# Kernel tuning notes

Hardware: AMD Instinct MI355X
Metric: run time of the kernel (lower is better)

Reference implementation:

```python
import jax, jax.numpy as jnp
import numpy as np

BETA = 1e-8
ALPHA = 0.5
CHOOSE_K = 128
MEMORY_SIZE = 65536
KEY_DIM = 256
BATCH = 1024


def _l2norm(x, axis=-1, eps=1e-12):
    return x / jnp.sqrt(jnp.sum(x * x, axis=axis, keepdims=True) + eps)


def setup_inputs() -> dict:
    key = jax.random.key(0)
    k1, k2, k3 = jax.random.split(key, 3)
    q = _l2norm(jax.random.normal(k1, (BATCH, KEY_DIM), dtype=jnp.float32))
    memory_key = _l2norm(jax.random.normal(k2, (MEMORY_SIZE, KEY_DIM), dtype=jnp.float32))
    # module init: hist[:] = 1e-5; add small random variation so topk is non-degenerate
    memory_hist = 1e-5 + 1e-3 * jax.random.uniform(k3, (MEMORY_SIZE,), dtype=jnp.float32)
    # module init: values = ones, second half zeroed
    memory_values = jnp.concatenate([
        jnp.ones((MEMORY_SIZE // 2,), dtype=jnp.float32),
        jnp.zeros((MEMORY_SIZE - MEMORY_SIZE // 2,), dtype=jnp.float32),
    ])
    return {"q": q, "memory_key": memory_key,
            "memory_hist": memory_hist, "memory_values": memory_values}


def reference(q, memory_key, memory_hist, memory_values):
    # obtain_topk over FULL memory: dense similarity [B, M]
    sims = jnp.matmul(q, memory_key.T)                      # [B, M]
    scores = jnp.exp(sims - 1.0) * (memory_hist + BETA)[None, :]
    _, k_idxs = jax.lax.top_k(scores, CHOOSE_K)             # [B, K]

    # gather reduced memory at topk indices
    red_keys = memory_key[k_idxs]                           # [B, K, D]
    red_hist = memory_hist[k_idxs] * ALPHA                  # [B, K]
    red_vals = memory_values[k_idxs]                        # [B, K]

    # posterior over the K gathered slots
    sim_k = jnp.einsum('bd,bkd->bk', q, red_keys)           # [B, K]
    joint = jnp.exp(sim_k - 1.0) * (red_hist + BETA)        # [B, K]
    posterior = joint / jnp.sum(joint, axis=1, keepdims=True)
    result = jnp.sum(posterior * red_vals, axis=1)          # [B]
    return result
```

## Files before the change

kernel.cpp:

```cpp
#include <hip/hip_runtime.h>

#define BATCH   1024
#define MSIZE   65536
#define KDIM    256
#define CHOOSEK 128
#define SELK    160
#define CLCAP   2816
#define BETA    1e-8f
#define ALPHA   0.5f
#define KSC  425.0f
#define KOFF 7.2f

typedef short bf16x8 __attribute__((ext_vector_type(8)));
typedef float f32x4  __attribute__((ext_vector_type(4)));

__device__ inline unsigned int pack2bf(float a, float b) {
    unsigned int ua = __float_as_uint(a);
    unsigned int ub = __float_as_uint(b);
    ua += 0x7fffu + ((ua >> 16) & 1u);
    ub += 0x7fffu + ((ub >> 16) & 1u);
    return (ua >> 16) | (ub & 0xffff0000u);
}

#define GLD16(g, l) __builtin_amdgcn_global_load_lds( \
    (const __attribute__((address_space(1))) unsigned int*)(g), \
    (__attribute__((address_space(3))) unsigned int*)(l), 16, 0, 0)

__global__ __launch_bounds__(256)
void convert_kernel(const float* __restrict__ q, const float* __restrict__ key,
                    const float* __restrict__ hist,
                    unsigned short* __restrict__ qs, unsigned short* __restrict__ kb,
                    float* __restrict__ Ltab)
{
    const int bid = blockIdx.x, tid = threadIdx.x;
    if (bid < 8192) {
        const int off = bid * 256 + tid;
        const float4* s4 = (const float4*)key;
        float4 a = s4[off * 2], b = s4[off * 2 + 1];
        ((uint4*)kb)[off] = make_uint4(pack2bf(a.x, a.y), pack2bf(a.z, a.w),
                                       pack2bf(b.x, b.y), pack2bf(b.z, b.w));
    } else if (bid < 8320) {
        const int f = (bid - 8192) * 256 + tid;
        const int l = f & 63, j = (f >> 6) & 3, ks = (f >> 8) & 7;
        const int wmg = (f >> 11) & 3, bt = (f >> 13) & 3;
        const int r = bt * 256 + wmg * 64 + j * 16 + (l & 15);
        const int c = ks * 32 + (l >> 4) * 8;
        const float* src = q + (size_t)r * KDIM + c;
        float4 a = *(const float4*)src, b = *(const float4*)(src + 4);
        ((uint4*)qs)[f] = make_uint4(pack2bf(a.x, a.y), pack2bf(a.z, a.w),
                                     pack2bf(b.x, b.y), pack2bf(b.z, b.w));
    } else {
        const int n = (bid - 8320) * 256 + tid;
        Ltab[n] = (logf(hist[n] + BETA) + KOFF) * KSC;
    }
}

__global__ __launch_bounds__(512, 4)
void score_kernel(const unsigned short* __restrict__ qs,
                  const unsigned short* __restrict__ kb,
                  const float* __restrict__ Ltab,
                  unsigned char* __restrict__ s8,
                  unsigned long long* __restrict__ gmask)
{
    __shared__ __align__(16) unsigned short Bs[3][128 * 32];
    const int tid = threadIdx.x;
    const int bid = blockIdx.x;
    const int bt = (bid >> 3) & 3;
    const int b0 = bt * 256;
    const int n0 = ((bid & 7) + ((bid >> 5) << 3)) * 128;
    const int lane = tid & 63, wave = tid >> 6;
    const int wm = (wave >> 1) * 64, wn = (wave & 1) * 64;
    const int l15 = lane & 15, l4 = lane >> 4;
    const int wmg = wave >> 1;

    f32x4 acc[4][4] = {};

    const int srow = tid >> 2;
    const int seg  = (tid & 3) * 8;
    const unsigned short* gB = kb + (size_t)(n0 + srow) * KDIM + seg;
    const int lofs = srow * 32 + seg;

    const bf16x8* qw = (const bf16x8*)qs + (size_t)((bt * 4 + wmg) * 32) * 64 + lane;

    bf16x8 qf[2][4];

#define STAGE_B(st) GLD16(gB + (st) * 32, &Bs[(st) % 3][lofs])

#define STEP(s, WN) do {                                                          \
    asm volatile("s_waitcnt vmcnt(" #WN ")" ::: "memory");                        \
    __builtin_amdgcn_s_barrier();                                                 \
    asm volatile("" ::: "memory");                                                \
    if ((s) < 7) {                                                                \
        _Pragma("unroll")                                                         \
        for (int j = 0; j < 4; ++j)                                               \
            qf[((s) + 1) & 1][j] = qw[(((s) + 1) * 4 + j) * 64];                  \
    }                                                                             \
    if ((s) + 2 < 8) STAGE_B((s) + 2);                                            \
    bf16x8 kf[4];                                                                 \
    _Pragma("unroll")                                                             \
    for (int i = 0; i < 4; ++i)                                                   \
        kf[i] = *(const bf16x8*)(&Bs[(s) % 3][(wn + i * 16 + l15) * 32 + l4 * 8]);\
    __builtin_amdgcn_s_setprio(1);                                                \
    _Pragma("unroll")                                                             \
    for (int i = 0; i < 4; ++i)                                                   \
        _Pragma("unroll")                                                         \
        for (int j = 0; j < 4; ++j)                                               \
            acc[i][j] = __builtin_amdgcn_mfma_f32_16x16x32_bf16(kf[i], qf[(s) & 1][j], acc[i][j], 0, 0, 0); \
    __builtin_amdgcn_s_setprio(0);                                                \
} while (0)

#pragma unroll
    for (int j = 0; j < 4; ++j) qf[0][j] = qw[j * 64];
    STAGE_B(0); STAGE_B(1);

    STEP(0, 1); STEP(1, 1); STEP(2, 1); STEP(3, 1);
    STEP(4, 1); STEP(5, 1); STEP(6, 1); STEP(7, 0);

#undef STEP
#undef STAGE_B

    float4 Lv[4];
#pragma unroll
    for (int i = 0; i < 4; ++i)
        Lv[i] = *(const float4*)&Ltab[n0 + wn + i * 16 + l4 * 4];
#pragma unroll
    for (int j = 0; j < 4; ++j) {
        const int rb = b0 + wm + j * 16 + l15;
        const size_t row = (size_t)rb * MSIZE;
        unsigned int mlo = 0, mhi = 0;
#pragma unroll
        for (int i = 0; i < 4; ++i) {
            const float* lv = (const float*)&Lv[i];
            const int nb = n0 + wn + i * 16 + l4 * 4;
            unsigned int pk = 0;
#pragma unroll
            for (int reg = 0; reg < 4; ++reg) {
                float x = fmaf(acc[i][j][reg], KSC, lv[reg]);
                x = fminf(fmaxf(x, 0.0f), 255.0f);
                pk |= (unsigned int)(int)x << (8 * reg);
            }
            *(unsigned int*)(s8 + row + nb) = pk;
            unsigned int nib = ((pk >> 7) & 1u) | ((pk >> 14) & 2u) |
                               ((pk >> 21) & 4u) | ((pk >> 28) & 8u);
            if (i < 2) mlo |= nib << (i * 16 + l4 * 4);
            else       mhi |= nib << ((i - 2) * 16 + l4 * 4);
        }
        mlo |= __shfl_xor(mlo, 16, 64); mhi |= __shfl_xor(mhi, 16, 64);
        mlo |= __shfl_xor(mlo, 32, 64); mhi |= __shfl_xor(mhi, 32, 64);
        if (l4 == 0)
            gmask[(size_t)rb * (MSIZE / 64) + ((n0 + wn) >> 6)] =
                ((unsigned long long)mhi << 32) | mlo;
    }
}

__global__ __launch_bounds__(256, 4)
void select_kernel(const float* __restrict__ q,
                   const float* __restrict__ key,
                   const float* __restrict__ hist,
                   const float* __restrict__ vals,
                   const unsigned char* __restrict__ s8,
                   const unsigned long long* __restrict__ gmask,
                   float* __restrict__ out)
{
    const int b   = blockIdx.x;
    const int tid = threadIdx.x;

    __shared__ __align__(16) float qs[KDIM];
    __shared__ unsigned int hcnt[8 * 257];
    __shared__ int   stot[256];
    __shared__ int   scal[3];
    __shared__ unsigned int clist[CLCAP];
    __shared__ int   cidx[1024];
    __shared__ float csc[1024], cjj[1024], cjv[1024];
    __shared__ float wred[8];

    qs[tid] = q[(size_t)b * KDIM + tid];
    const unsigned char* s8row = s8 + (size_t)b * MSIZE;
    const unsigned long long* gm = gmask + (size_t)b * (MSIZE / 64);
    const int rep = (tid & 7) * 257;

    for (int i = tid; i < 8 * 257; i += 256) hcnt[i] = 0u;
    if (tid == 0) { scal[0] = -1; scal[1] = 0; scal[2] = 0; }
    __syncthreads();

    for (int k = tid; k < MSIZE / 64; k += 256) {
        unsigned long long m = gm[k];
        while (m) {
            int bpos = __builtin_ctzll(m);
            m &= m - 1;
            int idx = k * 64 + bpos;
            unsigned int by = s8row[idx];
            int p = atomicAdd(&scal[2], 1);
            if (p < CLCAP) clist[p] = (by << 16) | (unsigned int)idx;
            atomicAdd(&hcnt[rep + by], 1u);
        }
    }
    __syncthreads();
    const int ncl = scal[2];
    int mode = (ncl >= SELK && ncl <= CLCAP) ? 0 : 1;
    int H = -1;

    for (;;) {
        if (mode == 1) {
            __syncthreads();
            for (int i = tid; i < 8 * 257; i += 256) hcnt[i] = 0u;
            if (tid == 0) { scal[0] = -1; scal[1] = 0; }
            __syncthreads();
            const uint4* rowp = reinterpret_cast<const uint4*>(s8row);
            for (int i = 0; i < 16; ++i) {
                uint4 v = rowp[i * 256 + tid];
                unsigned int w[4] = {v.x, v.y, v.z, v.w};
#pragma unroll
                for (int k = 0; k < 4; ++k)
#pragma unroll
                    for (int jj = 0; jj < 4; ++jj)
                        atomicAdd(&hcnt[rep + ((w[k] >> (8 * jj)) & 0xffu)], 1u);
            }
            __syncthreads();
        }
        { unsigned int t = 0;
#pragma unroll
          for (int k = 0; k < 8; ++k) t += hcnt[k * 257 + tid];
          stot[tid] = (int)t; }
        __syncthreads();
        if (tid < 64) {
            const int l = tid;
            int t0 = stot[l * 4], t1 = stot[l * 4 + 1], t2 = stot[l * 4 + 2], t3 = stot[l * 4 + 3];
            int lsum = t0 + t1 + t2 + t3;
            int s = lsum;
#pragma unroll
            for (int off = 1; off < 64; off <<= 1) {
                int u = __shfl_down(s, off, 64);
                if (l + off < 64) s += u;
            }
            int A  = s - lsum;
            int S3 = A + t3;
            int S2 = S3 + t2;
            int S1 = S2 + t1;
            int S0 = S1 + t0;
            if (S0 >= SELK && S1 < SELK) scal[0] = l * 4 + 0;
            if (S1 >= SELK && S2 < SELK) scal[0] = l * 4 + 1;
            if (S2 >= SELK && S3 < SELK) scal[0] = l * 4 + 2;
            if (S3 >= SELK && A  < SELK) scal[0] = l * 4 + 3;
        }
        __syncthreads();
        H = scal[0];
        __syncthreads();
        if (H >= 0) break;
        mode = 1;
    }

    const unsigned int uH = (unsigned int)H;
    if (mode == 0) {
        for (int i = tid; i < ncl; i += 256) {
            unsigned int e = clist[i];
            if ((e >> 16) >= uH) {
                int p = atomicAdd(&scal[1], 1);
                if (p < 1024) cidx[p] = (int)(e & 0xffffu);
            }
        }
    } else {
        const uint4* rowp = reinterpret_cast<const uint4*>(s8row);
        for (int i = 0; i < 16; ++i) {
            uint4 v = rowp[i * 256 + tid];
            const int base = (i * 256 + tid) * 16;
            unsigned int w[4] = {v.x, v.y, v.z, v.w};
#pragma unroll
            for (int k = 0; k < 4; ++k)
#pragma unroll
                for (int jj = 0; jj < 4; ++jj) {
                    unsigned int bb = (w[k] >> (8 * jj)) & 0xffu;
                    if (bb >= uH) {
                        int p = atomicAdd(&scal[1], 1);
                        if (p < 1024) cidx[p] = base + 4 * k + jj;
                    }
                }
        }
    }
    __syncthreads();
    const int ncand = min(scal[1], 1024);

    const int gid = tid >> 4, gll = tid & 15;
    const float4* q4 = (const float4*)qs;
    for (int i = gid; i < ncand; i += 16) {
        const int idx = cidx[i];
        const float4* kp = (const float4*)(key + (size_t)idx * KDIM);
        float p = 0.f;
#pragma unroll
        for (int u = 0; u < 4; ++u) {
            float4 kk = kp[gll * 4 + u];
            float4 qq = q4[gll * 4 + u];
            p += kk.x * qq.x + kk.y * qq.y + kk.z * qq.z + kk.w * qq.w;
        }
#pragma unroll
        for (int off = 1; off < 16; off <<= 1) p += __shfl_xor(p, off, 64);
        if (gll == 0) {
            float e = expf(p - 1.0f);
            float h = hist[idx];
            csc[i] = e * (h + BETA);
            float j = e * (ALPHA * h + BETA);
            cjj[i] = j;
            cjv[i] = j * vals[idx];
        }
    }
    __syncthreads();

    const int wave = tid >> 6, lane = tid & 63;
    float pn = 0.f, pd = 0.f;
    for (int i = tid; i < ncand; i += 256) {
        float si = csc[i]; int ii = cidx[i]; int rank = 0;
        for (int t = 0; t < ncand; ++t) {
            float st = csc[t];
            rank += (st > si || (st == si && cidx[t] < ii)) ? 1 : 0;
        }
        if (rank < CHOOSEK) { pn += cjv[i]; pd += cjj[i]; }
    }
#pragma unroll
    for (int off = 32; off > 0; off >>= 1) {
        pn += __shfl_xor(pn, off, 64);
        pd += __shfl_xor(pd, off, 64);
    }
    if (lane == 0) { wred[wave] = pn; wred[4 + wave] = pd; }
    __syncthreads();
    if (tid == 0) {
        float n = wred[0] + wred[1] + wred[2] + wred[3];
        float d = wred[4] + wred[5] + wred[6] + wred[7];
        out[b] = n / d;
    }
}

extern "C" void kernel_launch(void* const* d_in, const int* in_sizes, int n_in,
                              void* d_out, int out_size, void* d_ws, size_t ws_size,
                              hipStream_t stream)
{
    (void)in_sizes; (void)n_in; (void)out_size; (void)ws_size;
    const float* q    = (const float*)d_in[0];
    const float* key  = (const float*)d_in[1];
    const float* hist = (const float*)d_in[2];
    const float* vals = (const float*)d_in[3];
    float* out = (float*)d_out;

    unsigned char*  s8 = (unsigned char*)d_ws;
    unsigned short* kb = (unsigned short*)((char*)d_ws + ((size_t)64 << 20));
    unsigned short* qsw= (unsigned short*)((char*)d_ws + ((size_t)96 << 20));
    float*          Lt = (float*)((char*)d_ws + ((size_t)96 << 20) + (512 << 10));
    unsigned long long* gmask = (unsigned long long*)((char*)d_ws + ((size_t)97 << 20));

    convert_kernel<<<8576, 256, 0, stream>>>(q, key, hist, qsw, kb, Lt);
    score_kernel<<<2048, 512, 0, stream>>>(qsw, kb, Lt, s8, gmask);
    select_kernel<<<BATCH, 256, 0, stream>>>(q, key, hist, vals, s8, gmask, out);
}
```

Baseline: 203.7 us.

## Process two N-tiles per score block, overlapping first epilogue with second tile prefetch

Each score_kernel block now handles two consecutive 128-column tiles of memory keys instead of one, halving the grid to 1024 blocks. The 3-stage LDS pipeline continues across the tile boundary, so the first tile's epilogue (byte quantization and mask writes) runs while loads for the second tile are already in flight. This is meant to amortize block launch and pipeline fill/drain costs, at the expense of fewer blocks for load balancing and some added register pressure.

```diff
diff --git a/kernel.cpp b/kernel.cpp
--- a/kernel.cpp
+++ b/kernel.cpp
@@ -67,7 +67,7 @@
     const int bid = blockIdx.x;
     const int bt = (bid >> 3) & 3;
     const int b0 = bt * 256;
-    const int n0 = ((bid & 7) + ((bid >> 5) << 3)) * 128;
+    const int n0 = ((bid & 7) + ((bid >> 5) << 3)) * 256;
     const int lane = tid & 63, wave = tid >> 6;
     const int wm = (wave >> 1) * 64, wn = (wave & 1) * 64;
     const int l15 = lane & 15, l4 = lane >> 4;
@@ -84,18 +84,19 @@
 
     bf16x8 qf[2][4];
 
-#define STAGE_B(st) GLD16(gB + (st) * 32, &Bs[(st) % 3][lofs])
+#define STAGE_B(st) GLD16(gB + ((st) >> 3) * 128 * KDIM + ((st) & 7) * 32, \
+                          &Bs[(st) % 3][lofs])
 
 #define STEP(s, WN) do {                                                          \
     asm volatile("s_waitcnt vmcnt(" #WN ")" ::: "memory");                        \
     __builtin_amdgcn_s_barrier();                                                 \
     asm volatile("" ::: "memory");                                                \
-    if ((s) < 7) {                                                                \
+    if ((s) < 15) {                                                               \
         _Pragma("unroll")                                                         \
         for (int j = 0; j < 4; ++j)                                               \
-            qf[((s) + 1) & 1][j] = qw[(((s) + 1) * 4 + j) * 64];                  \
+            qf[((s) + 1) & 1][j] = qw[((((s) + 1) & 7) * 4 + j) * 64];            \
     }                                                                             \
-    if ((s) + 2 < 8) STAGE_B((s) + 2);                                            \
+    if ((s) + 2 < 16) STAGE_B((s) + 2);                                           \
     bf16x8 kf[4];                                                                 \
     _Pragma("unroll")                                                             \
     for (int i = 0; i < 4; ++i)                                                   \
@@ -109,48 +110,64 @@
     __builtin_amdgcn_s_setprio(0);                                                \
 } while (0)
 
+#define EPI(T) do {                                                               \
+    float4 Lv[4];                                                                 \
+    _Pragma("unroll")                                                             \
+    for (int i = 0; i < 4; ++i)                                                   \
+        Lv[i] = *(const float4*)&Ltab[n0 + (T) * 128 + wn + i * 16 + l4 * 4];     \
+    _Pragma("unroll")                                                             \
+    for (int j = 0; j < 4; ++j) {                                                 \
+        const int rb = b0 + wm + j * 16 + l15;                                    \
+        const size_t row = (size_t)rb * MSIZE;                                    \
+        unsigned int mlo = 0, mhi = 0;                                            \
+        _Pragma("unroll")                                                         \
+        for (int i = 0; i < 4; ++i) {                                             \
+            const float* lv = (const float*)&Lv[i];                               \
+            const int nb = n0 + (T) * 128 + wn + i * 16 + l4 * 4;                 \
+            unsigned int pk = 0;                                                  \
+            _Pragma("unroll")                                                     \
+            for (int reg = 0; reg < 4; ++reg) {                                   \
+                float x = fmaf(acc[i][j][reg], KSC, lv[reg]);                     \
+                x = fminf(fmaxf(x, 0.0f), 255.0f);                                \
+                pk |= (unsigned int)(int)x << (8 * reg);                          \
+            }                                                                     \
+            *(unsigned int*)(s8 + row + nb) = pk;                                 \
+            unsigned int nib = ((pk >> 7) & 1u) | ((pk >> 14) & 2u) |             \
+                               ((pk >> 21) & 4u) | ((pk >> 28) & 8u);             \
+            if (i < 2) mlo |= nib << (i * 16 + l4 * 4);                           \
+            else       mhi |= nib << ((i - 2) * 16 + l4 * 4);                     \
+        }                                                                         \
+        mlo |= __shfl_xor(mlo, 16, 64); mhi |= __shfl_xor(mhi, 16, 64);           \
+        mlo |= __shfl_xor(mlo, 32, 64); mhi |= __shfl_xor(mhi, 32, 64);           \
+        if (l4 == 0)                                                              \
+            gmask[(size_t)rb * (MSIZE / 64) + ((n0 + (T) * 128 + wn) >> 6)] =     \
+                ((unsigned long long)mhi << 32) | mlo;                            \
+    }                                                                             \
+} while (0)
+
 #pragma unroll
     for (int j = 0; j < 4; ++j) qf[0][j] = qw[j * 64];
     STAGE_B(0); STAGE_B(1);
 
     STEP(0, 1); STEP(1, 1); STEP(2, 1); STEP(3, 1);
-    STEP(4, 1); STEP(5, 1); STEP(6, 1); STEP(7, 0);
-
+    STEP(4, 1); STEP(5, 1); STEP(6, 1); STEP(7, 1);
+
+    EPI(0);
+#pragma unroll
+    for (int i = 0; i < 4; ++i)
+#pragma unroll
+        for (int j = 0; j < 4; ++j)
+            acc[i][j] = (f32x4){0.f, 0.f, 0.f, 0.f};
+
+    STEP(8, 2);
+    STEP(9, 1); STEP(10, 1); STEP(11, 1); STEP(12, 1);
+    STEP(13, 1); STEP(14, 1); STEP(15, 0);
+
+    EPI(1);
+
+#undef EPI
 #undef STEP
 #undef STAGE_B
-
-    float4 Lv[4];
-#pragma unroll
-    for (int i = 0; i < 4; ++i)
-        Lv[i] = *(const float4*)&Ltab[n0 + wn + i * 16 + l4 * 4];
-#pragma unroll
-    for (int j = 0; j < 4; ++j) {
-        const int rb = b0 + wm + j * 16 + l15;
-        const size_t row = (size_t)rb * MSIZE;
-        unsigned int mlo = 0, mhi = 0;
-#pragma unroll
-        for (int i = 0; i < 4; ++i) {
-            const float* lv = (const float*)&Lv[i];
-            const int nb = n0 + wn + i * 16 + l4 * 4;
-            unsigned int pk = 0;
-#pragma unroll
-            for (int reg = 0; reg < 4; ++reg) {
-                float x = fmaf(acc[i][j][reg], KSC, lv[reg]);
-                x = fminf(fmaxf(x, 0.0f), 255.0f);
-                pk |= (unsigned int)(int)x << (8 * reg);
-            }
-            *(unsigned int*)(s8 + row + nb) = pk;
-            unsigned int nib = ((pk >> 7) & 1u) | ((pk >> 14) & 2u) |
-                               ((pk >> 21) & 4u) | ((pk >> 28) & 8u);
-            if (i < 2) mlo |= nib << (i * 16 + l4 * 4);
-            else       mhi |= nib << ((i - 2) * 16 + l4 * 4);
-        }
-        mlo |= __shfl_xor(mlo, 16, 64); mhi |= __shfl_xor(mhi, 16, 64);
-        mlo |= __shfl_xor(mlo, 32, 64); mhi |= __shfl_xor(mhi, 32, 64);
-        if (l4 == 0)
-            gmask[(size_t)rb * (MSIZE / 64) + ((n0 + wn) >> 6)] =
-                ((unsigned long long)mhi << 32) | mlo;
-    }
 }
 
 __global__ __launch_bounds__(256, 4)
@@ -347,6 +364,6 @@
     unsigned long long* gmask = (unsigned long long*)((char*)d_ws + ((size_t)97 << 20));
 
     convert_kernel<<<8576, 256, 0, stream>>>(q, key, hist, qsw, kb, Lt);
-    score_kernel<<<2048, 512, 0, stream>>>(qsw, kb, Lt, s8, gmask);
+    score_kernel<<<1024, 512, 0, stream>>>(qsw, kb, Lt, s8, gmask);
     select_kernel<<<BATCH, 256, 0, stream>>>(q, key, hist, vals, s8, gmask, out);
 }
```

After: 257.6 us. 26.5% more time.

## Use fixed-threshold bitmask directly as candidate list, skipping histogram in common path

Applied to the files above, without the earlier changes.

The GEMM epilogue now sets mask bits for quantized scores at or above a fixed threshold instead of the top bit. The select kernel counts mask bits with popcount and a wave reduction. When the count falls between SELK and 1024, it writes candidate indices straight from the mask using a per-thread atomic offset, with no byte histogram, threshold search or clist compaction. This cuts shared-memory atomics and a byte read per candidate. It relies on the fixed threshold giving a suitable candidate count and falls back to the full histogram path otherwise.

```diff
diff --git a/kernel.cpp b/kernel.cpp
--- a/kernel.cpp
+++ b/kernel.cpp
@@ -5,7 +5,7 @@
 #define KDIM    256
 #define CHOOSEK 128
 #define SELK    160
-#define CLCAP   2816
+#define MASKT   152
 #define BETA    1e-8f
 #define ALPHA   0.5f
 #define KSC  425.0f
@@ -132,16 +132,15 @@
         for (int i = 0; i < 4; ++i) {
             const float* lv = (const float*)&Lv[i];
             const int nb = n0 + wn + i * 16 + l4 * 4;
-            unsigned int pk = 0;
+            unsigned int pk = 0, nib = 0;
 #pragma unroll
             for (int reg = 0; reg < 4; ++reg) {
                 float x = fmaf(acc[i][j][reg], KSC, lv[reg]);
                 x = fminf(fmaxf(x, 0.0f), 255.0f);
                 pk |= (unsigned int)(int)x << (8 * reg);
+                nib |= (x >= (float)MASKT ? 1u : 0u) << reg;
             }
             *(unsigned int*)(s8 + row + nb) = pk;
-            unsigned int nib = ((pk >> 7) & 1u) | ((pk >> 14) & 2u) |
-                               ((pk >> 21) & 4u) | ((pk >> 28) & 8u);
             if (i < 2) mlo |= nib << (i * 16 + l4 * 4);
             else       mhi |= nib << ((i - 2) * 16 + l4 * 4);
         }
@@ -168,8 +167,7 @@
     __shared__ __align__(16) float qs[KDIM];
     __shared__ unsigned int hcnt[8 * 257];
     __shared__ int   stot[256];
-    __shared__ int   scal[3];
-    __shared__ unsigned int clist[CLCAP];
+    __shared__ int   scal[4];
     __shared__ int   cidx[1024];
     __shared__ float csc[1024], cjj[1024], cjv[1024];
     __shared__ float wred[8];
@@ -177,47 +175,51 @@
     qs[tid] = q[(size_t)b * KDIM + tid];
     const unsigned char* s8row = s8 + (size_t)b * MSIZE;
     const unsigned long long* gm = gmask + (size_t)b * (MSIZE / 64);
-    const int rep = (tid & 7) * 257;
-
-    for (int i = tid; i < 8 * 257; i += 256) hcnt[i] = 0u;
-    if (tid == 0) { scal[0] = -1; scal[1] = 0; scal[2] = 0; }
+
+    if (tid == 0) { scal[0] = -1; scal[1] = 0; scal[2] = 0; scal[3] = 0; }
     __syncthreads();
 
-    for (int k = tid; k < MSIZE / 64; k += 256) {
-        unsigned long long m = gm[k];
-        while (m) {
-            int bpos = __builtin_ctzll(m);
-            m &= m - 1;
-            int idx = k * 64 + bpos;
-            unsigned int by = s8row[idx];
-            int p = atomicAdd(&scal[2], 1);
-            if (p < CLCAP) clist[p] = (by << 16) | (unsigned int)idx;
-            atomicAdd(&hcnt[rep + by], 1u);
-        }
-    }
+    unsigned long long mw[4];
+    int myc = 0;
+#pragma unroll
+    for (int k = 0; k < 4; ++k) { mw[k] = gm[tid + k * 256]; myc += __popcll(mw[k]); }
+    { int ws = myc;
+#pragma unroll
+      for (int off = 32; off > 0; off >>= 1) ws += __shfl_xor(ws, off, 64);
+      if ((tid & 63) == 0) atomicAdd((unsigned int*)&scal[2], (unsigned int)ws); }
     __syncthreads();
-    const int ncl = scal[2];
-    int mode = (ncl >= SELK && ncl <= CLCAP) ? 0 : 1;
-    int H = -1;
-
-    for (;;) {
-        if (mode == 1) {
-            __syncthreads();
-            for (int i = tid; i < 8 * 257; i += 256) hcnt[i] = 0u;
-            if (tid == 0) { scal[0] = -1; scal[1] = 0; }
-            __syncthreads();
-            const uint4* rowp = reinterpret_cast<const uint4*>(s8row);
-            for (int i = 0; i < 16; ++i) {
-                uint4 v = rowp[i * 256 + tid];
-                unsigned int w[4] = {v.x, v.y, v.z, v.w};
-#pragma unroll
-                for (int k = 0; k < 4; ++k)
-#pragma unroll
-                    for (int jj = 0; jj < 4; ++jj)
-                        atomicAdd(&hcnt[rep + ((w[k] >> (8 * jj)) & 0xffu)], 1u);
+    const int cntB = scal[2];
+    const int mode = (cntB >= SELK && cntB <= 1024) ? 0 : 1;
+    int ncand;
+
+    if (mode == 0) {
+        int base = atomicAdd(&scal[1], myc);
+#pragma unroll
+        for (int k = 0; k < 4; ++k) {
+            unsigned long long m = mw[k];
+            while (m) {
+                int bpos = __builtin_ctzll(m);
+                m &= m - 1;
+                cidx[base++] = (tid + k * 256) * 64 + bpos;
             }
-            __syncthreads();
-        }
+        }
+        ncand = cntB;
+        __syncthreads();
+    } else {
+        const uint4* rowp = reinterpret_cast<const uint4*>(s8row);
+        const int rep = (tid & 7) * 257;
+        for (int i = tid; i < 8 * 257; i += 256) hcnt[i] = 0u;
+        __syncthreads();
+        for (int i = 0; i < 16; ++i) {
+            uint4 v = rowp[i * 256 + tid];
+            unsigned int w[4] = {v.x, v.y, v.z, v.w};
+#pragma unroll
+            for (int k = 0; k < 4; ++k)
+#pragma unroll
+                for (int jj = 0; jj < 4; ++jj)
+                    atomicAdd(&hcnt[rep + ((w[k] >> (8 * jj)) & 0xffu)], 1u);
+        }
+        __syncthreads();
         { unsigned int t = 0;
 #pragma unroll
           for (int k = 0; k < 8; ++k) t += hcnt[k * 257 + tid];
@@ -234,33 +236,15 @@
                 if (l + off < 64) s += u;
             }
             int A  = s - lsum;
-            int S3 = A + t3;
-            int S2 = S3 + t2;
-            int S1 = S2 + t1;
-            int S0 = S1 + t0;
+            int S3 = A + t3, S2 = S3 + t2, S1 = S2 + t1, S0 = S1 + t0;
             if (S0 >= SELK && S1 < SELK) scal[0] = l * 4 + 0;
             if (S1 >= SELK && S2 < SELK) scal[0] = l * 4 + 1;
             if (S2 >= SELK && S3 < SELK) scal[0] = l * 4 + 2;
             if (S3 >= SELK && A  < SELK) scal[0] = l * 4 + 3;
         }
         __syncthreads();
-        H = scal[0];
-        __syncthreads();
-        if (H >= 0) break;
-        mode = 1;
-    }
-
-    const unsigned int uH = (unsigned int)H;
-    if (mode == 0) {
-        for (int i = tid; i < ncl; i += 256) {
-            unsigned int e = clist[i];
-            if ((e >> 16) >= uH) {
-                int p = atomicAdd(&scal[1], 1);
-                if (p < 1024) cidx[p] = (int)(e & 0xffffu);
-            }
-        }
-    } else {
-        const uint4* rowp = reinterpret_cast<const uint4*>(s8row);
+        const int H = (scal[0] >= 0) ? scal[0] : 0;
+        const unsigned int uH = (unsigned int)H;
         for (int i = 0; i < 16; ++i) {
             uint4 v = rowp[i * 256 + tid];
             const int base = (i * 256 + tid) * 16;
@@ -271,14 +255,14 @@
                 for (int jj = 0; jj < 4; ++jj) {
                     unsigned int bb = (w[k] >> (8 * jj)) & 0xffu;
                     if (bb >= uH) {
-                        int p = atomicAdd(&scal[1], 1);
+                        int p = atomicAdd(&scal[3], 1);
                         if (p < 1024) cidx[p] = base + 4 * k + jj;
                     }
                 }
         }
-    }
-    __syncthreads();
-    const int ncand = min(scal[1], 1024);
+        __syncthreads();
+        ncand = min(scal[3], 1024);
+    }
 
     const int gid = tid >> 4, gll = tid & 15;
     const float4* q4 = (const float4*)qs;
```

New measurement: 274.5 us. +34.7%, slower.
